# Kernel optimization log

Hardware: AMD Instinct MI355X
Metric: run time of the kernel (lower is better)

## Reference

```python
import jax, jax.numpy as jnp
import numpy as np

B, S, G, C = 4, 512, 48, 12
D = G * C            # d_model = 576, divisible by nhead=3
N = B * S * G        # 98304 graph nodes
E = N * 16           # 1572864 edges
H, FF = 3, 2048
HD = D // H
SCALE = 1.0 / float(np.sqrt(HD))


def _leaky(x):
    return jnp.where(x > 0, x, 0.2 * x)


def _ln(x, g, b):
    m = jnp.mean(x, -1, keepdims=True)
    v = jnp.var(x, -1, keepdims=True)
    return (x - m) * jax.lax.rsqrt(v + 1e-5) * g + b


def _conv(x, w, b, stride=1):
    # x: [B, Cin, L], w: [Cout, Cin, K]
    y = jax.lax.conv_general_dilated(x, w, (stride,), 'SAME',
                                     dimension_numbers=('NCH', 'OIH', 'NCH'))
    return y + b[None, :, None]


def _gat(x, src, dst, W, a_s, a_d, bias):
    # single-head GATConv (PyG defaults: self-loops already in src/dst, leaky 0.2)
    xp = x @ W.T                                            # [N, C]
    e = _leaky((xp @ a_s)[src] + (xp @ a_d)[dst])           # [E+N]
    m = jax.ops.segment_max(e, dst, num_segments=N)
    w = jnp.exp(e - m[dst])
    denom = jax.ops.segment_sum(w, dst, num_segments=N)
    alpha = w / denom[dst]
    return jax.ops.segment_sum(alpha[:, None] * xp[src], dst, num_segments=N) + bias


def _forward(edge_index, x, mask, noise,
             W_enc, a_src_enc, a_dst_enc, b_enc,
             Wq, bq, Wk, bk, Wv, bv, Wo, bo,
             ln1_g, ln1_b, W1, b1, W2, b2, ln2_g, ln2_b,
             enc1_w, enc1_b, down_w, down_b, bott_w, bott_b,
             up_w, up_b, dec_w, dec_b,
             W_dec, a_src_dec, a_dst_dec, b_dec):
    loops = jnp.arange(N)
    src = jnp.concatenate([edge_index[0], loops])
    dst = jnp.concatenate([edge_index[1], loops])
    # masked blend of observed data and imputation noise
    h = x * mask + noise * (1.0 - mask)
    h = _gat(h, src, dst, W_enc, a_src_enc, a_dst_enc, b_enc)       # [N, C]
    t = h.reshape(B, S, D)
    # TransformerEncoderLayer (post-norm, relu FFN, 3 heads)
    q = (t @ Wq.T + bq).reshape(B, S, H, HD)
    k = (t @ Wk.T + bk).reshape(B, S, H, HD)
    v = (t @ Wv.T + bv).reshape(B, S, H, HD)
    att = jax.nn.softmax(jnp.einsum('bqhd,bkhd->bhqk', q, k) * SCALE, axis=-1)
    o = jnp.einsum('bhqk,bkhd->bqhd', att, v).reshape(B, S, D) @ Wo.T + bo
    t = _ln(t + o, ln1_g, ln1_b)
    ff = jax.nn.relu(t @ W1.T + b1) @ W2.T + b2
    t = _ln(t + ff, ln2_g, ln2_b)
    # Unet1d auto-encoder over the time axis, channels = D
    y = t.transpose(0, 2, 1)                                        # [B, D, S]
    e1 = jax.nn.relu(_conv(y, enc1_w, enc1_b))                      # [B, D, S]
    d1 = jax.nn.relu(_conv(e1, down_w, down_b, 2))                  # [B, 2D, S/2]
    bt = jax.nn.relu(_conv(d1, bott_w, bott_b))                     # [B, 2D, S/2]
    up = jax.nn.relu(_conv(jnp.repeat(bt, 2, axis=2), up_w, up_b))  # [B, D, S]
    y = _conv(jnp.concatenate([up, e1], axis=1), dec_w, dec_b)      # [B, D, S]
    # GAT decoder + tanh
    h = y.transpose(0, 2, 1).reshape(N, C)
    h = _gat(h, src, dst, W_dec, a_src_dec, a_dst_dec, b_dec)
    return jnp.tanh(h)


def setup_inputs() -> dict:
    ks = iter(jax.random.split(jax.random.key(0), 64))
    def nrm(shape, s=0.2):
        return jax.random.normal(next(ks), shape, jnp.float32) * s
    return dict(
        edge_index=jax.random.randint(next(ks), (2, E), 0, N),
        x=jax.random.normal(next(ks), (N, C), jnp.float32),
        mask=(jax.random.uniform(next(ks), (N, C)) < 0.8).astype(jnp.float32),
        noise=jax.random.normal(next(ks), (N, C), jnp.float32),
        W_enc=nrm((C, C)), a_src_enc=nrm((C,)), a_dst_enc=nrm((C,)), b_enc=jnp.zeros((C,), jnp.float32),
        Wq=nrm((D, D), 0.05), bq=jnp.zeros((D,)), Wk=nrm((D, D), 0.05), bk=jnp.zeros((D,)),
        Wv=nrm((D, D), 0.05), bv=jnp.zeros((D,)), Wo=nrm((D, D), 0.05), bo=jnp.zeros((D,)),
        ln1_g=jnp.ones((D,)), ln1_b=jnp.zeros((D,)),
        W1=nrm((FF, D), 0.05), b1=jnp.zeros((FF,)), W2=nrm((D, FF), 0.05), b2=jnp.zeros((D,)),
        ln2_g=jnp.ones((D,)), ln2_b=jnp.zeros((D,)),
        enc1_w=nrm((D, D, 3), 0.03), enc1_b=jnp.zeros((D,)),
        down_w=nrm((2 * D, D, 3), 0.03), down_b=jnp.zeros((2 * D,)),
        bott_w=nrm((2 * D, 2 * D, 3), 0.02), bott_b=jnp.zeros((2 * D,)),
        up_w=nrm((D, 2 * D, 3), 0.02), up_b=jnp.zeros((D,)),
        dec_w=nrm((D, 2 * D, 3), 0.02), dec_b=jnp.zeros((D,)),
        W_dec=nrm((C, C)), a_src_dec=nrm((C,)), a_dst_dec=nrm((C,)), b_dec=jnp.zeros((C,), jnp.float32),
    )


def reference(edge_index, x, mask, noise,
              W_enc, a_src_enc, a_dst_enc, b_enc,
              Wq, bq, Wk, bk, Wv, bv, Wo, bo,
              ln1_g, ln1_b, W1, b1, W2, b2, ln2_g, ln2_b,
              enc1_w, enc1_b, down_w, down_b, bott_w, bott_b,
              up_w, up_b, dec_w, dec_b,
              W_dec, a_src_dec, a_dst_dec, b_dec):
    return _forward(edge_index, x, mask, noise,
                    W_enc, a_src_enc, a_dst_enc, b_enc,
                    Wq, bq, Wk, bk, Wv, bv, Wo, bo,
                    ln1_g, ln1_b, W1, b1, W2, b2, ln2_g, ln2_b,
                    enc1_w, enc1_b, down_w, down_b, bott_w, bott_b,
                    up_w, up_b, dec_w, dec_b,
                    W_dec, a_src_dec, a_dst_dec, b_dec)
```

## Files before the change

kernel.cpp:

```cpp
#include <hip/hip_runtime.h>
#include <hip/hip_bf16.h>
#include <math.h>

#define NN 98304
#define CC 12
#define EE 1572864
#define ETOT (EE + NN)
#define BB 4
#define SS 512
#define DD 576
#define HH 3
#define HDI 192
#define FFD 2048
#define MR (BB*SS)
#define ND (NN*CC)
#define ATT_SCALE 0.07216878364870323f
#define NB 768
#define BCAP 2560
#define BINB2 512
#define CHUNK2 3264

typedef __hip_bfloat16 bf;
typedef __attribute__((ext_vector_type(8))) short s8v;
typedef __attribute__((ext_vector_type(4))) short s4v;
typedef __attribute__((ext_vector_type(4))) float f4v;

__device__ __forceinline__ void gl16(const void* g, void* l) {
    __builtin_amdgcn_global_load_lds(
        (const __attribute__((address_space(1))) unsigned int*)g,
        (__attribute__((address_space(3))) unsigned int*)l, 16, 0, 0);
}
__device__ __forceinline__ short bfbits(float f) {
    bf t = __float2bfloat16(f);
    return *(short*)&t;
}
__device__ __forceinline__ unsigned pk2(float a, float b) {
    return (unsigned)(unsigned short)bfbits(a) |
           ((unsigned)(unsigned short)bfbits(b) << 16);
}
__device__ __forceinline__ float lo16(unsigned v) { return __uint_as_float(v << 16); }
__device__ __forceinline__ float hi16(unsigned v) { return __uint_as_float(v & 0xffff0000u); }

__global__ __launch_bounds__(256) void gat_node_k(
    const float* __restrict__ xin, const float* __restrict__ mask,
    const float* __restrict__ noise,
    const float* __restrict__ W, const float* __restrict__ a_s,
    const float* __restrict__ a_d,
    float4* __restrict__ rows, float* __restrict__ dval,
    int blend)
{
    int n = blockIdx.x * 256 + threadIdx.x;
    if (n >= NN) return;
    const float4* xr = (const float4*)(xin + (size_t)n*CC);
    float h[CC];
    float4 h0 = xr[0], h1 = xr[1], h2 = xr[2];
    h[0]=h0.x; h[1]=h0.y; h[2]=h0.z; h[3]=h0.w;
    h[4]=h1.x; h[5]=h1.y; h[6]=h1.z; h[7]=h1.w;
    h[8]=h2.x; h[9]=h2.y; h[10]=h2.z; h[11]=h2.w;
    if (blend) {
        const float4* mr = (const float4*)(mask  + (size_t)n*CC);
        const float4* nr = (const float4*)(noise + (size_t)n*CC);
        float m[CC], z[CC];
        float4 m0=mr[0],m1=mr[1],m2=mr[2], z0=nr[0],z1=nr[1],z2=nr[2];
        m[0]=m0.x;m[1]=m0.y;m[2]=m0.z;m[3]=m0.w;m[4]=m1.x;m[5]=m1.y;m[6]=m1.z;m[7]=m1.w;
        m[8]=m2.x;m[9]=m2.y;m[10]=m2.z;m[11]=m2.w;
        z[0]=z0.x;z[1]=z0.y;z[2]=z0.z;z[3]=z0.w;z[4]=z1.x;z[5]=z1.y;z[6]=z1.z;z[7]=z1.w;
        z[8]=z2.x;z[9]=z2.y;z[10]=z2.z;z[11]=z2.w;
#pragma unroll
        for (int c = 0; c < CC; ++c) h[c] = h[c]*m[c] + z[c]*(1.0f-m[c]);
    }
    float sv = 0.f, dv = 0.f;
    float o[CC];
#pragma unroll
    for (int oc = 0; oc < CC; ++oc) {
        float a = 0.f;
#pragma unroll
        for (int ic = 0; ic < CC; ++ic) a += h[ic]*W[oc*CC+ic];
        o[oc] = a;
        sv += a * a_s[oc]; dv += a * a_d[oc];
    }
    float4 r0, r1;
    r0.x = sv;
    r0.y = __uint_as_float(pk2(o[0], o[1]));
    r0.z = __uint_as_float(pk2(o[2], o[3]));
    r0.w = __uint_as_float(pk2(o[4], o[5]));
    r1.x = __uint_as_float(pk2(o[6], o[7]));
    r1.y = __uint_as_float(pk2(o[8], o[9]));
    r1.z = __uint_as_float(pk2(o[10], o[11]));
    r1.w = 0.f;
    rows[(size_t)n*2]   = r0;
    rows[(size_t)n*2+1] = r1;
    dval[n] = dv;
}

__global__ __launch_bounds__(256) void binA1_k(
    const int* __restrict__ e1, int* __restrict__ gcnt)
{
    __shared__ int lh[NB];
    const int tid = threadIdx.x;
    const int lo = blockIdx.x * CHUNK2, hi = lo + CHUNK2;
    for (int b = tid; b < NB; b += 256) lh[b] = 0;
    __syncthreads();
    for (int i = lo + tid; i < hi; i += 256) {
        int d = (i < EE) ? e1[i] : (i - EE);
        atomicAdd(&lh[d >> 7], 1);
    }
    __syncthreads();
    for (int b = tid; b < NB; b += 256)
        gcnt[(size_t)blockIdx.x*NB + b] = lh[b];
}

__global__ __launch_bounds__(512) void binscan_k(
    const int* __restrict__ gcnt, int* __restrict__ gbase, int* __restrict__ bcnt)
{
    __shared__ int sh[BINB2];
    const int b = blockIdx.x, t = threadIdx.x;
    int v = gcnt[(size_t)t*NB + b];
    sh[t] = v; __syncthreads();
    for (int off = 1; off < BINB2; off <<= 1) {
        int add = (t >= off) ? sh[t-off] : 0;
        __syncthreads();
        sh[t] += add;
        __syncthreads();
    }
    gbase[(size_t)b*BINB2 + t] = sh[t] - v;
    if (t == BINB2-1) bcnt[b] = sh[BINB2-1];
}

__global__ __launch_bounds__(256) void binA2_k(
    const int* __restrict__ e0, const int* __restrict__ e1,
    const int* __restrict__ gbase, unsigned* __restrict__ pairs)
{
    __shared__ int lbase[NB];
    __shared__ int lh[NB];
    const int tid = threadIdx.x;
    const int lo = blockIdx.x * CHUNK2, hi = lo + CHUNK2;
    for (int b = tid; b < NB; b += 256) {
        lbase[b] = gbase[(size_t)b*BINB2 + blockIdx.x];
        lh[b] = 0;
    }
    __syncthreads();
    for (int i = lo + tid; i < hi; i += 256) {
        int s, d;
        if (i < EE) { s = e0[i]; d = e1[i]; }
        else        { s = i - EE; d = s; }
        int b = d >> 7;
        int p = lbase[b] + atomicAdd(&lh[b], 1);
        if (p < BCAP)
            pairs[(size_t)b*BCAP + p] = ((unsigned)(d & 127) << 17) | (unsigned)s;
    }
}

__global__ __launch_bounds__(1024) void binB_k(
    unsigned* __restrict__ pairs, const int* __restrict__ bcnt,
    int* __restrict__ cnt, int* __restrict__ offs)
{
    __shared__ unsigned ent[BCAP];
    __shared__ int lh[128], ls[128], lc[128];
    const int b = blockIdx.x, tid = threadIdx.x;
    const int n = min(bcnt[b], BCAP);
    for (int i = tid; i < n; i += 1024) ent[i] = pairs[(size_t)b*BCAP + i];
    if (tid < 128) lh[tid] = 0;
    __syncthreads();
    for (int i = tid; i < n; i += 1024) atomicAdd(&lh[ent[i] >> 17], 1);
    __syncthreads();
    if (tid == 0) { int run = 0; for (int j = 0; j < 128; ++j) { ls[j] = run; run += lh[j]; } }
    __syncthreads();
    if (tid < 128) {
        int node = b*128 + tid;
        cnt[node]  = lh[tid];
        offs[node] = b*BCAP + ls[tid];
        lc[tid]    = ls[tid];
    }
    __syncthreads();
    for (int i = tid; i < n; i += 1024) {
        unsigned v = ent[i];
        int dl = (int)(v >> 17);
        int p = atomicAdd(&lc[dl], 1);
        pairs[(size_t)b*BCAP + p] = v & 0x1FFFFu;
    }
}

__global__ __launch_bounds__(256) void gat_agg8_k(
    const unsigned* __restrict__ pairs, const int* __restrict__ cnt,
    const int* __restrict__ offs,
    const float4* __restrict__ rows, const float* __restrict__ dval,
    const float* __restrict__ bias,
    float* __restrict__ out, bf* __restrict__ outb, int dotanh)
{
    int g = blockIdx.x*32 + (threadIdx.x >> 3);
    int l = threadIdx.x & 7;
    if (g >= NN) return;
    int beg = offs[g], m = cnt[g];
    float dv = dval[g];
    float acc[CC] = {};
    float den = 0.f;
    for (int i = l; i < m; i += 8) {
        unsigned s = pairs[beg + i];
        float4 r0 = rows[(size_t)s*2];
        float4 r1 = rows[(size_t)s*2+1];
        float e = r0.x + dv;
        e = e > 0.f ? e : 0.2f*e;
        float w = __expf(e);
        den += w;
        unsigned p01 = __float_as_uint(r0.y), p23 = __float_as_uint(r0.z);
        unsigned p45 = __float_as_uint(r0.w), p67 = __float_as_uint(r1.x);
        unsigned p89 = __float_as_uint(r1.y), pab = __float_as_uint(r1.z);
        acc[0]  += w*lo16(p01); acc[1]  += w*hi16(p01);
        acc[2]  += w*lo16(p23); acc[3]  += w*hi16(p23);
        acc[4]  += w*lo16(p45); acc[5]  += w*hi16(p45);
        acc[6]  += w*lo16(p67); acc[7]  += w*hi16(p67);
        acc[8]  += w*lo16(p89); acc[9]  += w*hi16(p89);
        acc[10] += w*lo16(pab); acc[11] += w*hi16(pab);
    }
#pragma unroll
    for (int off = 1; off < 8; off <<= 1) {
        den += __shfl_xor(den, off);
#pragma unroll
        for (int c = 0; c < CC; ++c) acc[c] += __shfl_xor(acc[c], off);
    }
    if (l == 0) {
        float inv = 1.f / den;
        float r[CC];
#pragma unroll
        for (int c = 0; c < CC; ++c) {
            r[c] = acc[c]*inv + bias[c];
            if (dotanh) r[c] = tanhf(r[c]);
        }
        if (out) {
            float4* orow = (float4*)(out + (size_t)g*CC);
            orow[0] = make_float4(r[0],r[1],r[2],r[3]);
            orow[1] = make_float4(r[4],r[5],r[6],r[7]);
            orow[2] = make_float4(r[8],r[9],r[10],r[11]);
        }
        if (outb) {
            s4v* brow = (s4v*)(outb + (size_t)g*CC);
            s4v b0, b1, b2;
            b0[0]=bfbits(r[0]); b0[1]=bfbits(r[1]); b0[2]=bfbits(r[2]); b0[3]=bfbits(r[3]);
            b1[0]=bfbits(r[4]); b1[1]=bfbits(r[5]); b1[2]=bfbits(r[6]); b1[3]=bfbits(r[7]);
            b2[0]=bfbits(r[8]); b2[1]=bfbits(r[9]); b2[2]=bfbits(r[10]); b2[3]=bfbits(r[11]);
            brow[0]=b0; brow[1]=b1; brow[2]=b2;
        }
    }
}

template<int TBM>
__global__ __launch_bounds__(256) void gemm_bt(
    const bf* __restrict__ A, const bf* __restrict__ B,
    const float* __restrict__ bias, float* __restrict__ Cf, bf* __restrict__ Cb,
    int K, int lda, int ldb, int ldc,
    long long sA1, long long sA2, long long sB1, long long sB2,
    long long sC1, long long sC2, int bdiv, long long sBias,
    float scale, int relu, int vtmode)
{
    constexpr int MI = TBM/32;
    __shared__ bf As[TBM*32];
    __shared__ bf Bs[64*32];
    const int tid = threadIdx.x, lane = tid & 63, wave = tid >> 6;
    const int z = blockIdx.z, z1 = z / bdiv, z2 = z % bdiv;
    const bf* Ab = A + z1*sA1 + z2*sA2;
    const bf* Bb = B + z1*sB1 + z2*sB2;
    const int bm = blockIdx.y * TBM, bn = blockIdx.x * 64;
    const int l4 = lane >> 2;
    const int swz0 = (l4 >> 1) & 3;
    const int lc = (((lane & 3) ^ swz0) * 8);
    const int arow0 = wave*(TBM/4) + l4;
    const int brow  = wave*16 + l4;
    const int wm = wave >> 1, wn = wave & 1;
    const int fr = lane & 15;
    const int gsw = (((lane >> 4) ^ ((fr >> 1) & 3)) * 8);
    f4v acc[MI][2] = {};

    for (int k0 = 0; k0 < K; k0 += 32) {
        gl16(Ab + (size_t)(bm + arow0)*lda + k0 + lc, As + wave*(TBM/4)*32);
        if constexpr (TBM == 128)
            gl16(Ab + (size_t)(bm + arow0 + 16)*lda + k0 + lc, As + wave*1024 + 512);
        gl16(Bb + (size_t)(bn + brow )*ldb + k0 + lc, Bs + wave*512);
        __syncthreads();
        s8v af[MI], bfv[2];
#pragma unroll
        for (int mi = 0; mi < MI; ++mi)
            af[mi] = *(const s8v*)&As[(wm*(TBM/2) + mi*16 + fr)*32 + gsw];
#pragma unroll
        for (int nj = 0; nj < 2; ++nj)
            bfv[nj] = *(const s8v*)&Bs[(wn*32 + nj*16 + fr)*32 + gsw];
#pragma unroll
        for (int mi = 0; mi < MI; ++mi)
#pragma unroll
            for (int nj = 0; nj < 2; ++nj)
                acc[mi][nj] = __builtin_amdgcn_mfma_f32_16x16x32_bf16(
                    af[mi], bfv[nj], acc[mi][nj], 0, 0, 0);
        __syncthreads();
    }

    const float* bp = bias ? bias + z1*sBias : nullptr;
    if (vtmode && z1 == 2) {
        bf* vt = Cb + 2*sC1;
#pragma unroll
        for (int mi = 0; mi < MI; ++mi) {
#pragma unroll
            for (int nj = 0; nj < 2; ++nj) {
                int col = bn + wn*32 + nj*16 + fr;
                float bv = bp ? bp[col] : 0.f;
                int row0 = bm + wm*(TBM/2) + mi*16 + (lane>>4)*4;
                int b = row0 >> 9, s0 = row0 & 511;
                int h = col / HDI, dd = col - h*HDI;
                s4v pk;
#pragma unroll
                for (int r = 0; r < 4; ++r)
                    pk[r] = bfbits(acc[mi][nj][r] + bv);
                *(s4v*)&vt[((size_t)((b*HH + h)*HDI + dd))*SS + s0] = pk;
            }
        }
        return;
    }
    float* Cfb = Cf ? Cf + z1*sC1 + z2*sC2 : nullptr;
    bf*    Cbb = Cb ? Cb + z1*sC1 + z2*sC2 : nullptr;
#pragma unroll
    for (int mi = 0; mi < MI; ++mi) {
#pragma unroll
        for (int nj = 0; nj < 2; ++nj) {
            int col = bn + wn*32 + nj*16 + fr;
            float bv = bp ? bp[col] : 0.f;
#pragma unroll
            for (int r = 0; r < 4; ++r) {
                int row = bm + wm*(TBM/2) + mi*16 + (lane>>4)*4 + r;
                float vv = (acc[mi][nj][r] + bv) * scale;
                if (relu) vv = fmaxf(vv, 0.f);
                if (Cfb) Cfb[(size_t)row*ldc + col] = vv;
                if (Cbb) Cbb[(size_t)row*ldc + col] = __float2bfloat16(vv);
            }
        }
    }
}

template<int CIN, int MODE>
__global__ __launch_bounds__(256) void conv_bt(
    const bf* __restrict__ A0, const bf* __restrict__ A1,
    const bf* __restrict__ Bw, float* __restrict__ Cpart,
    int K, int M, int N, int Lout, int Lin, int splitk)
{
    __shared__ bf As[64*32];
    __shared__ bf Bs[64*32];
    const int tid = threadIdx.x, lane = tid & 63, wave = tid >> 6;
    const int bm = blockIdx.y * 64, bn = blockIdx.x * 64;
    const int kchunk = K / splitk;
    const int kbeg = blockIdx.z * kchunk, kend = kbeg + kchunk;
    const int l4 = lane >> 2;
    const int swz0 = (l4 >> 1) & 3;
    const int lc = (((lane & 3) ^ swz0) * 8);
    const int arow = bm + wave*16 + l4;
    const int brow = bn + wave*16 + l4;
    const int ab = arow / Lout, al = arow % Lout;
    const int wm = wave >> 1, wn = wave & 1;
    const int fr = lane & 15;
    const int gsw = (((lane >> 4) ^ ((fr >> 1) & 3)) * 8);
    f4v acc[2][2] = {};

    for (int k0 = kbeg; k0 < kend; k0 += 32) {
        int kk  = k0 / CIN;
        int ci0 = k0 - kk*CIN;
        int row;
        if constexpr (MODE == 1)      row = 2*al + kk + 1;
        else if constexpr (MODE == 2) row = (al + kk + 1) >> 1;
        else                          row = al + kk;
        const bf* src;
        if constexpr (MODE == 3) {
            constexpr int CH = CIN/2;
            bool lohalf = ci0 < CH;
            src = (lohalf ? A0 : A1)
                + ((size_t)(ab*(Lin+2) + row))*CH + (lohalf ? ci0 : ci0 - CH);
        } else {
            src = A0 + ((size_t)(ab*(Lin+2) + row))*CIN + ci0;
        }
        gl16(src + lc, As + wave*512);
        gl16(Bw + (size_t)brow*K + k0 + lc, Bs + wave*512);
        __syncthreads();
        s8v af[2], bfv[2];
#pragma unroll
        for (int mi = 0; mi < 2; ++mi)
            af[mi] = *(const s8v*)&As[(wm*32 + mi*16 + fr)*32 + gsw];
#pragma unroll
        for (int nj = 0; nj < 2; ++nj)
            bfv[nj] = *(const s8v*)&Bs[(wn*32 + nj*16 + fr)*32 + gsw];
#pragma unroll
        for (int mi = 0; mi < 2; ++mi)
#pragma unroll
            for (int nj = 0; nj < 2; ++nj)
                acc[mi][nj] = __builtin_amdgcn_mfma_f32_16x16x32_bf16(
                    af[mi], bfv[nj], acc[mi][nj], 0, 0, 0);
        __syncthreads();
    }

    float* Cp = Cpart + (size_t)blockIdx.z * M * N;
#pragma unroll
    for (int mi = 0; mi < 2; ++mi)
#pragma unroll
        for (int nj = 0; nj < 2; ++nj) {
            int col = bn + wn*32 + nj*16 + fr;
#pragma unroll
            for (int r = 0; r < 4; ++r) {
                int row = bm + wm*32 + mi*16 + (lane>>4)*4 + r;
                Cp[(size_t)row*N + col] = acc[mi][nj][r];
            }
        }
}

__global__ __launch_bounds__(256) void convepi_k(
    const float* __restrict__ part, const float* __restrict__ bias,
    bf* __restrict__ outb, float* __restrict__ outf,
    int M, int N, int Lout, int relu, int nsplit)
{
    int total = M * (N >> 3);
    int i = blockIdx.x*256 + threadIdx.x;
    if (i >= total) return;
    int c8 = (i % (N >> 3)) * 8;
    int row = i / (N >> 3);
    float v[8];
#pragma unroll
    for (int j = 0; j < 8; ++j) v[j] = bias[c8+j];
    for (int z = 0; z < nsplit; ++z) {
        const float* p = part + (size_t)z*M*N + (size_t)row*N + c8;
#pragma unroll
        for (int j = 0; j < 8; ++j) v[j] += p[j];
    }
    if (relu) {
#pragma unroll
        for (int j = 0; j < 8; ++j) v[j] = fmaxf(v[j], 0.f);
    }
    if (outb) {
        int b = row / Lout, l = row % Lout;
        s8v pk;
#pragma unroll
        for (int j = 0; j < 8; ++j) pk[j] = bfbits(v[j]);
        *(s8v*)&outb[((size_t)(b*(Lout+2) + l + 1))*N + c8] = pk;
    }
    if (outf) {
        float4* o = (float4*)(outf + (size_t)row*N + c8);
        o[0] = make_float4(v[0],v[1],v[2],v[3]);
        o[1] = make_float4(v[4],v[5],v[6],v[7]);
    }
}

struct PJob { int type; const float* src; void* dst; int a; int b; };
struct PJobs { PJob j[14]; };
__global__ __launch_bounds__(256) void prep_k(PJobs J)
{
    PJob jb = J.j[blockIdx.y];
    if (jb.type == 0) {
        for (int i = blockIdx.x*256 + threadIdx.x; i < jb.a; i += gridDim.x*256) {
            float4 v = ((const float4*)jb.src)[i];
            s4v p;
            p[0]=bfbits(v.x); p[1]=bfbits(v.y); p[2]=bfbits(v.z); p[3]=bfbits(v.w);
            ((s4v*)jb.dst)[i] = p;
        }
    } else if (jb.type == 1) {
        for (int i = blockIdx.x*256 + threadIdx.x; i < jb.a; i += gridDim.x*256)
            ((float4*)jb.dst)[i] = ((const float4*)jb.src)[i];
    } else {
        int n8 = BB * 2 * (jb.b >> 3);
        for (int i = blockIdx.x*256 + threadIdx.x; i < n8; i += gridDim.x*256) {
            int c8 = i % (jb.b >> 3); int r = i / (jb.b >> 3);
            int bb = r >> 1; int row = (r & 1) ? (jb.a + 1) : 0;
            s8v z = {0,0,0,0,0,0,0,0};
            *(s8v*)&((bf*)jb.dst)[((size_t)(bb*(jb.a+2) + row))*jb.b + c8*8] = z;
        }
    }
}

struct WJob { const float* w; bf* wT; int Cout; int Cin; };
struct WJobs { WJob j[5]; };
__global__ __launch_bounds__(256) void wtrans5_k(WJobs J)
{
    WJob jb = J.j[blockIdx.y];
    int n8 = jb.Cout * 3 * (jb.Cin >> 3);
    for (int i = blockIdx.x*256 + threadIdx.x; i < n8; i += gridDim.x*256) {
        int c8 = i % (jb.Cin >> 3); int r = i / (jb.Cin >> 3);
        int kk = r % 3; int co = r / 3;
        int ci = c8 * 8;
        s8v ov;
#pragma unroll
        for (int j = 0; j < 8; ++j)
            ov[j] = bfbits(jb.w[((size_t)co*jb.Cin + ci + j)*3 + kk]);
        *(s8v*)&jb.wT[(size_t)co*3*jb.Cin + (size_t)kk*jb.Cin + ci] = ov;
    }
}

__global__ __launch_bounds__(256) void softmax_k(
    const float* __restrict__ S, bf* __restrict__ P)
{
    int row = blockIdx.x; size_t base = (size_t)row * SS;
    int tid = threadIdx.x;
    __shared__ float red[256];
    float v0 = S[base+tid], v1 = S[base+tid+256];
    red[tid] = fmaxf(v0, v1); __syncthreads();
    for (int off = 128; off > 0; off >>= 1) {
        if (tid < off) red[tid] = fmaxf(red[tid], red[tid+off]);
        __syncthreads();
    }
    float mx = red[0]; __syncthreads();
    float e0 = __expf(v0-mx), e1 = __expf(v1-mx);
    red[tid] = e0+e1; __syncthreads();
    for (int off = 128; off > 0; off >>= 1) {
        if (tid < off) red[tid] += red[tid+off];
        __syncthreads();
    }
    float inv = 1.f / red[0];
    P[base+tid]     = __float2bfloat16(e0*inv);
    P[base+tid+256] = __float2bfloat16(e1*inv);
}

__global__ __launch_bounds__(256) void ln_k(
    const float* __restrict__ a, const float* __restrict__ r,
    const float* __restrict__ g, const float* __restrict__ be,
    float* __restrict__ out, bf* __restrict__ ob, int padout)
{
    int row = blockIdx.x; int tid = threadIdx.x;
    __shared__ float red[256], red2[256];
    size_t base = (size_t)row * DD;
    size_t base2 = padout ? ((size_t)(row + 2*(row/SS) + 1))*DD : base;
    float x0 = a[base+tid]      + r[base+tid];
    float x1 = a[base+tid+256]  + r[base+tid+256];
    float x2 = (tid < 64) ? (a[base+tid+512] + r[base+tid+512]) : 0.f;
    float s  = x0+x1+x2;
    float s2 = x0*x0 + x1*x1 + x2*x2;
    red[tid] = s; red2[tid] = s2; __syncthreads();
    for (int off = 128; off > 0; off >>= 1) {
        if (tid < off) { red[tid] += red[tid+off]; red2[tid] += red2[tid+off]; }
        __syncthreads();
    }
    float mean = red[0] / (float)DD;
    float var  = red2[0] / (float)DD - mean*mean;
    float inv = rsqrtf(var + 1e-5f);
    float y0 = (x0-mean)*inv*g[tid]     + be[tid];
    float y1 = (x1-mean)*inv*g[tid+256] + be[tid+256];
    if (out) { out[base+tid] = y0; out[base+tid+256] = y1; }
    if (ob)  { ob[base2+tid] = __float2bfloat16(y0); ob[base2+tid+256] = __float2bfloat16(y1); }
    if (tid < 64) {
        float y2 = (x2-mean)*inv*g[tid+512] + be[tid+512];
        if (out) out[base+tid+512] = y2;
        if (ob)  ob[base2+tid+512] = __float2bfloat16(y2);
    }
}

extern "C" void kernel_launch(void* const* d_in, const int* in_sizes, int n_in,
                              void* d_out, int out_size, void* d_ws, size_t ws_size,
                              hipStream_t stream)
{
    const int*   edge   = (const int*)  d_in[0];
    const float* x      = (const float*)d_in[1];
    const float* mask   = (const float*)d_in[2];
    const float* noise  = (const float*)d_in[3];
    const float* W_enc  = (const float*)d_in[4];
    const float* asrc_e = (const float*)d_in[5];
    const float* adst_e = (const float*)d_in[6];
    const float* b_enc  = (const float*)d_in[7];
    const float* Wq = (const float*)d_in[8];  const float* bq = (const float*)d_in[9];
    const float* Wk = (const float*)d_in[10]; const float* bk = (const float*)d_in[11];
    const float* Wv = (const float*)d_in[12]; const float* bv = (const float*)d_in[13];
    const float* Wo = (const float*)d_in[14]; const float* bo = (const float*)d_in[15];
    const float* ln1g = (const float*)d_in[16]; const float* ln1b = (const float*)d_in[17];
    const float* W1 = (const float*)d_in[18]; const float* b1 = (const float*)d_in[19];
    const float* W2 = (const float*)d_in[20]; const float* b2 = (const float*)d_in[21];
    const float* ln2g = (const float*)d_in[22]; const float* ln2b = (const float*)d_in[23];
    const float* enc1_w = (const float*)d_in[24]; const float* enc1_b = (const float*)d_in[25];
    const float* down_w = (const float*)d_in[26]; const float* down_b = (const float*)d_in[27];
    const float* bott_w = (const float*)d_in[28]; const float* bott_b = (const float*)d_in[29];
    const float* up_w   = (const float*)d_in[30]; const float* up_b   = (const float*)d_in[31];
    const float* dec_w  = (const float*)d_in[32]; const float* dec_b  = (const float*)d_in[33];
    const float* W_dec  = (const float*)d_in[34];
    const float* asrc_d = (const float*)d_in[35];
    const float* adst_d = (const float*)d_in[36];
    const float* b_dec  = (const float*)d_in[37];
    float* out = (float*)d_out;

    float* ws = (float*)d_ws;
    float4*   rows  = (float4*)ws;
    float*    dval  = ws + 786432;
    int*      cnt   = (int*)(ws + 884736);
    int*      offs  = (int*)(ws + 983040);
    unsigned* pairs = (unsigned*)(ws + 1376256);
    int*      bcnt  = (int*)(ws + 3342336);
    float*    t     = ws + 3343360;
    bf*       tb    = (bf*)(ws + 4523008);
    bf*       qb    = (bf*)(ws + 5112832);
    bf*       kb    = (bf*)(ws + 5702656);
    bf*       vb    = (bf*)(ws + 6292480);
    float*    big   = ws + 6882304;
    int*      gcnt  = (int*)big;
    int*      gbase = (int*)(big + 393216);
    float*    scores = big;
    bf*       Pb    = (bf*)(big + 3145728);
    bf*       wTbott = (bf*)big;
    float*    o     = ws + 11600896;
    float*    parts = ws + 11600896;
    float*    t1    = ws + 12780544;
    bf*       t1b   = (bf*)(ws + 13960192);
    bf*       ff1b  = (bf*)(ws + 14550016);
    bf*       t2p   = (bf*)(ws + 16647168);
    bf*       e1p   = (bf*)(ws + 17239296);
    bf*       d1p   = (bf*)(ws + 17831424);
    bf*       btbp  = (bf*)(ws + 18425856);
    bf*       upp   = (bf*)(ws + 19020288);
    float*    dec   = ws + 19612416;
    bf*       wTb   = (bf*)(ws + 20792064);
    bf*       Wqb   = (bf*)(ws + 21787392);
    bf*       Wkb   = (bf*)(ws + 21953280);
    bf*       Wvb   = (bf*)(ws + 22119168);
    bf*       Wob   = (bf*)(ws + 22285056);
    bf*       W1b   = (bf*)(ws + 22450944);
    bf*       W2b   = (bf*)(ws + 23040768);
    float*    biasQKV = ws + 23630592;
    bf*       vt    = vb;
    bf*       attnO = qb;
    bf*       wTenc  = wTb;
    bf*       wTdown = (bf*)t;
    bf*       wTup   = kb;
    bf*       wTdec  = tb;

    const int* e0 = edge;
    const int* e1i = edge + EE;

    binA1_k<<<BINB2, 256, 0, stream>>>(e1i, gcnt);
    binscan_k<<<NB, BINB2, 0, stream>>>(gcnt, gbase, bcnt);
    binA2_k<<<BINB2, 256, 0, stream>>>(e0, e1i, gbase, pairs);
    binB_k<<<NB, 1024, 0, stream>>>(pairs, bcnt, cnt, offs);

    {
        PJobs J;
        J.j[0]  = { 0, Wq, Wqb, DD*DD/4, 0 };
        J.j[1]  = { 0, Wk, Wkb, DD*DD/4, 0 };
        J.j[2]  = { 0, Wv, Wvb, DD*DD/4, 0 };
        J.j[3]  = { 0, Wo, Wob, DD*DD/4, 0 };
        J.j[4]  = { 0, W1, W1b, FFD*DD/4, 0 };
        J.j[5]  = { 0, W2, W2b, FFD*DD/4, 0 };
        J.j[6]  = { 1, bq, biasQKV,        DD/4, 0 };
        J.j[7]  = { 1, bk, biasQKV + DD,   DD/4, 0 };
        J.j[8]  = { 1, bv, biasQKV + 2*DD, DD/4, 0 };
        J.j[9]  = { 2, nullptr, t2p,  512, 576 };
        J.j[10] = { 2, nullptr, e1p,  512, 576 };
        J.j[11] = { 2, nullptr, d1p,  256, 1152 };
        J.j[12] = { 2, nullptr, btbp, 256, 1152 };
        J.j[13] = { 2, nullptr, upp,  512, 576 };
        prep_k<<<dim3(576, 14), 256, 0, stream>>>(J);
    }

    gat_node_k<<<NN/256, 256, 0, stream>>>(x, mask, noise, W_enc, asrc_e, adst_e,
                                           rows, dval, 1);
    gat_agg8_k<<<NN/32, 256, 0, stream>>>(pairs, cnt, offs, rows, dval, b_enc,
                                          t, tb, 0);

    gemm_bt<128><<<dim3(9,16,3), 256, 0, stream>>>(tb, Wqb, biasQKV, nullptr, qb,
        DD, DD, DD, DD,
        0,0, (long long)DD*DD,0, (long long)MR*DD,0, 1, DD, 1.f, 0, 1);
    gemm_bt<128><<<dim3(8,4,12), 256, 0, stream>>>(qb, kb, nullptr, scores, nullptr,
        HDI, DD, DD, SS,
        (long long)SS*DD, HDI, (long long)SS*DD, HDI,
        3LL*SS*SS, (long long)SS*SS, HH, 0, ATT_SCALE, 0, 0);
    softmax_k<<<12*SS, 256, 0, stream>>>(scores, Pb);
    gemm_bt<64><<<dim3(3,8,12), 256, 0, stream>>>(Pb, vt, nullptr, nullptr, attnO,
        SS, SS, SS, DD,
        3LL*SS*SS, (long long)SS*SS, 3LL*HDI*SS, (long long)HDI*SS,
        (long long)SS*DD, HDI, HH, 0, 1.f, 0, 0);
    gemm_bt<64><<<dim3(9,32,1), 256, 0, stream>>>(attnO, Wob, bo, o, nullptr,
        DD, DD, DD, DD, 0,0,0,0,0,0, 1, 0, 1.f, 0, 0);
    ln_k<<<MR, 256, 0, stream>>>(t, o, ln1g, ln1b, t1, t1b, 0);
    gemm_bt<128><<<dim3(32,16,1), 256, 0, stream>>>(t1b, W1b, b1, nullptr, ff1b,
        DD, DD, DD, FFD, 0,0,0,0,0,0, 1, 0, 1.f, 1, 0);
    gemm_bt<64><<<dim3(9,32,1), 256, 0, stream>>>(ff1b, W2b, b2, o, nullptr,
        FFD, FFD, FFD, DD, 0,0,0,0,0,0, 1, 0, 1.f, 0, 0);
    ln_k<<<MR, 256, 0, stream>>>(t1, o, ln2g, ln2b, nullptr, t2p, 1);

    {
        WJobs W5;
        W5.j[0] = { enc1_w, wTenc,  576,  576 };
        W5.j[1] = { down_w, wTdown, 1152, 576 };
        W5.j[2] = { bott_w, wTbott, 1152, 1152 };
        W5.j[3] = { up_w,   wTup,   576,  1152 };
        W5.j[4] = { dec_w,  wTdec,  576,  1152 };
        wtrans5_k<<<dim3(1024, 5), 256, 0, stream>>>(W5);
    }
    conv_bt<576,0><<<dim3(9,32,3), 256, 0, stream>>>(t2p, nullptr, wTenc, parts,
        1728, 2048, 576, 512, 512, 3);
    convepi_k<<<576, 256, 0, stream>>>(parts, enc1_b, e1p, nullptr, 2048, 576, 512, 1, 3);
    conv_bt<576,1><<<dim3(18,16,3), 256, 0, stream>>>(e1p, nullptr, wTdown, parts,
        1728, 1024, 1152, 256, 512, 3);
    convepi_k<<<576, 256, 0, stream>>>(parts, down_b, d1p, nullptr, 1024, 1152, 256, 1, 3);
    conv_bt<1152,0><<<dim3(18,16,4), 256, 0, stream>>>(d1p, nullptr, wTbott, parts,
        3456, 1024, 1152, 256, 256, 4);
    convepi_k<<<576, 256, 0, stream>>>(parts, bott_b, btbp, nullptr, 1024, 1152, 256, 1, 4);
    conv_bt<1152,2><<<dim3(9,32,4), 256, 0, stream>>>(btbp, nullptr, wTup, parts,
        3456, 2048, 576, 512, 256, 4);
    convepi_k<<<576, 256, 0, stream>>>(parts, up_b, upp, nullptr, 2048, 576, 512, 1, 4);
    conv_bt<1152,3><<<dim3(9,32,4), 256, 0, stream>>>(upp, e1p, wTdec, parts,
        3456, 2048, 576, 512, 512, 4);
    convepi_k<<<576, 256, 0, stream>>>(parts, dec_b, nullptr, dec, 2048, 576, 512, 0, 4);

    gat_node_k<<<NN/256, 256, 0, stream>>>(dec, nullptr, nullptr, W_dec, asrc_d, adst_d,
                                           rows, dval, 0);
    gat_agg8_k<<<NN/32, 256, 0, stream>>>(pairs, cnt, offs, rows, dval, b_dec,
                                          out, nullptr, 1);
}
```

Measured before the change: 353.2 us.

## Replace split-K conv GEMMs with 32-row tiles and fused bias/ReLU epilogue

The five Conv1d GEMMs drop split-K with float partial buffers and separate reduction/epilogue kernels. Each now runs as a single kernel over the full K with 32-row tiles, applying bias, ReLU and the bf16 padded store directly. The gemm_bt template also gains a 32-row tile variant, used for the attention PV, Wo and W2 GEMMs to raise block counts. This removes the partial-sum traffic and five launches, at the cost of half as many MFMAs per block and two idle waves during A-tile loads.

```diff
diff --git a/kernel.cpp b/kernel.cpp
--- a/kernel.cpp
+++ b/kernel.cpp
@@ -264,7 +264,7 @@
     const int l4 = lane >> 2;
     const int swz0 = (l4 >> 1) & 3;
     const int lc = (((lane & 3) ^ swz0) * 8);
-    const int arow0 = wave*(TBM/4) + l4;
+    const int arow0 = wave*((TBM==128)?32:16) + l4;
     const int brow  = wave*16 + l4;
     const int wm = wave >> 1, wn = wave & 1;
     const int fr = lane & 15;
@@ -272,9 +272,15 @@
     f4v acc[MI][2] = {};
 
     for (int k0 = 0; k0 < K; k0 += 32) {
-        gl16(Ab + (size_t)(bm + arow0)*lda + k0 + lc, As + wave*(TBM/4)*32);
-        if constexpr (TBM == 128)
+        if constexpr (TBM == 32) {
+            if (wave < 2)
+                gl16(Ab + (size_t)(bm + arow0)*lda + k0 + lc, As + wave*512);
+        } else if constexpr (TBM == 64) {
+            gl16(Ab + (size_t)(bm + arow0)*lda + k0 + lc, As + wave*512);
+        } else {
+            gl16(Ab + (size_t)(bm + arow0)*lda + k0 + lc, As + wave*1024);
             gl16(Ab + (size_t)(bm + arow0 + 16)*lda + k0 + lc, As + wave*1024 + 512);
+        }
         gl16(Bb + (size_t)(bn + brow )*ldb + k0 + lc, Bs + wave*512);
         __syncthreads();
         s8v af[MI], bfv[2];
@@ -335,17 +341,16 @@
 }
 
 template<int CIN, int MODE>
-__global__ __launch_bounds__(256) void conv_bt(
+__global__ __launch_bounds__(256) void conv32_k(
     const bf* __restrict__ A0, const bf* __restrict__ A1,
-    const bf* __restrict__ Bw, float* __restrict__ Cpart,
-    int K, int M, int N, int Lout, int Lin, int splitk)
-{
-    __shared__ bf As[64*32];
+    const bf* __restrict__ Bw, const float* __restrict__ bias,
+    bf* __restrict__ outb, float* __restrict__ outf,
+    int K, int N, int Lout, int Lin, int relu)
+{
+    __shared__ bf As[32*32];
     __shared__ bf Bs[64*32];
     const int tid = threadIdx.x, lane = tid & 63, wave = tid >> 6;
-    const int bm = blockIdx.y * 64, bn = blockIdx.x * 64;
-    const int kchunk = K / splitk;
-    const int kbeg = blockIdx.z * kchunk, kend = kbeg + kchunk;
+    const int bm = blockIdx.y * 32, bn = blockIdx.x * 64;
     const int l4 = lane >> 2;
     const int swz0 = (l4 >> 1) & 3;
     const int lc = (((lane & 3) ^ swz0) * 8);
@@ -355,90 +360,52 @@
     const int wm = wave >> 1, wn = wave & 1;
     const int fr = lane & 15;
     const int gsw = (((lane >> 4) ^ ((fr >> 1) & 3)) * 8);
-    f4v acc[2][2] = {};
-
-    for (int k0 = kbeg; k0 < kend; k0 += 32) {
+    f4v acc[2] = {};
+
+    for (int k0 = 0; k0 < K; k0 += 32) {
         int kk  = k0 / CIN;
         int ci0 = k0 - kk*CIN;
-        int row;
-        if constexpr (MODE == 1)      row = 2*al + kk + 1;
-        else if constexpr (MODE == 2) row = (al + kk + 1) >> 1;
-        else                          row = al + kk;
-        const bf* src;
-        if constexpr (MODE == 3) {
-            constexpr int CH = CIN/2;
-            bool lohalf = ci0 < CH;
-            src = (lohalf ? A0 : A1)
-                + ((size_t)(ab*(Lin+2) + row))*CH + (lohalf ? ci0 : ci0 - CH);
-        } else {
-            src = A0 + ((size_t)(ab*(Lin+2) + row))*CIN + ci0;
-        }
-        gl16(src + lc, As + wave*512);
+        if (wave < 2) {
+            int row;
+            if constexpr (MODE == 1)      row = 2*al + kk + 1;
+            else if constexpr (MODE == 2) row = (al + kk + 1) >> 1;
+            else                          row = al + kk;
+            const bf* src;
+            if constexpr (MODE == 3) {
+                constexpr int CH = CIN/2;
+                bool lohalf = ci0 < CH;
+                src = (lohalf ? A0 : A1)
+                    + ((size_t)(ab*(Lin+2) + row))*CH + (lohalf ? ci0 : ci0 - CH);
+            } else {
+                src = A0 + ((size_t)(ab*(Lin+2) + row))*CIN + ci0;
+            }
+            gl16(src + lc, As + wave*512);
+        }
         gl16(Bw + (size_t)brow*K + k0 + lc, Bs + wave*512);
         __syncthreads();
-        s8v af[2], bfv[2];
-#pragma unroll
-        for (int mi = 0; mi < 2; ++mi)
-            af[mi] = *(const s8v*)&As[(wm*32 + mi*16 + fr)*32 + gsw];
-#pragma unroll
-        for (int nj = 0; nj < 2; ++nj)
-            bfv[nj] = *(const s8v*)&Bs[(wn*32 + nj*16 + fr)*32 + gsw];
-#pragma unroll
-        for (int mi = 0; mi < 2; ++mi)
-#pragma unroll
-            for (int nj = 0; nj < 2; ++nj)
-                acc[mi][nj] = __builtin_amdgcn_mfma_f32_16x16x32_bf16(
-                    af[mi], bfv[nj], acc[mi][nj], 0, 0, 0);
-        __syncthreads();
-    }
-
-    float* Cp = Cpart + (size_t)blockIdx.z * M * N;
-#pragma unroll
-    for (int mi = 0; mi < 2; ++mi)
-#pragma unroll
-        for (int nj = 0; nj < 2; ++nj) {
-            int col = bn + wn*32 + nj*16 + fr;
-#pragma unroll
-            for (int r = 0; r < 4; ++r) {
-                int row = bm + wm*32 + mi*16 + (lane>>4)*4 + r;
-                Cp[(size_t)row*N + col] = acc[mi][nj][r];
+        s8v af = *(const s8v*)&As[(wm*16 + fr)*32 + gsw];
+        s8v b0 = *(const s8v*)&Bs[(wn*32 + fr)*32 + gsw];
+        s8v b1 = *(const s8v*)&Bs[(wn*32 + 16 + fr)*32 + gsw];
+        acc[0] = __builtin_amdgcn_mfma_f32_16x16x32_bf16(af, b0, acc[0], 0, 0, 0);
+        acc[1] = __builtin_amdgcn_mfma_f32_16x16x32_bf16(af, b1, acc[1], 0, 0, 0);
+        __syncthreads();
+    }
+
+#pragma unroll
+    for (int nj = 0; nj < 2; ++nj) {
+        int col = bn + wn*32 + nj*16 + fr;
+        float bv = bias[col];
+#pragma unroll
+        for (int r = 0; r < 4; ++r) {
+            int row = bm + wm*16 + (lane>>4)*4 + r;
+            float vv = acc[nj][r] + bv;
+            if (relu) vv = fmaxf(vv, 0.f);
+            if (outb) {
+                int b = row / Lout, l = row % Lout;
+                outb[((size_t)(b*(Lout+2) + l + 1))*N + col] = __float2bfloat16(vv);
             }
-        }
-}
-
-__global__ __launch_bounds__(256) void convepi_k(
-    const float* __restrict__ part, const float* __restrict__ bias,
-    bf* __restrict__ outb, float* __restrict__ outf,
-    int M, int N, int Lout, int relu, int nsplit)
-{
-    int total = M * (N >> 3);
-    int i = blockIdx.x*256 + threadIdx.x;
-    if (i >= total) return;
-    int c8 = (i % (N >> 3)) * 8;
-    int row = i / (N >> 3);
-    float v[8];
-#pragma unroll
-    for (int j = 0; j < 8; ++j) v[j] = bias[c8+j];
-    for (int z = 0; z < nsplit; ++z) {
-        const float* p = part + (size_t)z*M*N + (size_t)row*N + c8;
-#pragma unroll
-        for (int j = 0; j < 8; ++j) v[j] += p[j];
-    }
-    if (relu) {
-#pragma unroll
-        for (int j = 0; j < 8; ++j) v[j] = fmaxf(v[j], 0.f);
-    }
-    if (outb) {
-        int b = row / Lout, l = row % Lout;
-        s8v pk;
-#pragma unroll
-        for (int j = 0; j < 8; ++j) pk[j] = bfbits(v[j]);
-        *(s8v*)&outb[((size_t)(b*(Lout+2) + l + 1))*N + c8] = pk;
-    }
-    if (outf) {
-        float4* o = (float4*)(outf + (size_t)row*N + c8);
-        o[0] = make_float4(v[0],v[1],v[2],v[3]);
-        o[1] = make_float4(v[4],v[5],v[6],v[7]);
+            if (outf) outf[(size_t)row*N + col] = vv;
+        }
     }
 }
 
@@ -593,7 +560,6 @@
     bf*       Pb    = (bf*)(big + 3145728);
     bf*       wTbott = (bf*)big;
     float*    o     = ws + 11600896;
-    float*    parts = ws + 11600896;
     float*    t1    = ws + 12780544;
     bf*       t1b   = (bf*)(ws + 13960192);
     bf*       ff1b  = (bf*)(ws + 14550016);
@@ -658,16 +624,16 @@
         (long long)SS*DD, HDI, (long long)SS*DD, HDI,
         3LL*SS*SS, (long long)SS*SS, HH, 0, ATT_SCALE, 0, 0);
     softmax_k<<<12*SS, 256, 0, stream>>>(scores, Pb);
-    gemm_bt<64><<<dim3(3,8,12), 256, 0, stream>>>(Pb, vt, nullptr, nullptr, attnO,
+    gemm_bt<32><<<dim3(3,16,12), 256, 0, stream>>>(Pb, vt, nullptr, nullptr, attnO,
         SS, SS, SS, DD,
         3LL*SS*SS, (long long)SS*SS, 3LL*HDI*SS, (long long)HDI*SS,
         (long long)SS*DD, HDI, HH, 0, 1.f, 0, 0);
-    gemm_bt<64><<<dim3(9,32,1), 256, 0, stream>>>(attnO, Wob, bo, o, nullptr,
+    gemm_bt<32><<<dim3(9,64,1), 256, 0, stream>>>(attnO, Wob, bo, o, nullptr,
         DD, DD, DD, DD, 0,0,0,0,0,0, 1, 0, 1.f, 0, 0);
     ln_k<<<MR, 256, 0, stream>>>(t, o, ln1g, ln1b, t1, t1b, 0);
     gemm_bt<128><<<dim3(32,16,1), 256, 0, stream>>>(t1b, W1b, b1, nullptr, ff1b,
         DD, DD, DD, FFD, 0,0,0,0,0,0, 1, 0, 1.f, 1, 0);
-    gemm_bt<64><<<dim3(9,32,1), 256, 0, stream>>>(ff1b, W2b, b2, o, nullptr,
+    gemm_bt<32><<<dim3(9,64,1), 256, 0, stream>>>(ff1b, W2b, b2, o, nullptr,
         FFD, FFD, FFD, DD, 0,0,0,0,0,0, 1, 0, 1.f, 0, 0);
     ln_k<<<MR, 256, 0, stream>>>(t1, o, ln2g, ln2b, nullptr, t2p, 1);
 
@@ -680,21 +646,16 @@
         W5.j[4] = { dec_w,  wTdec,  576,  1152 };
         wtrans5_k<<<dim3(1024, 5), 256, 0, stream>>>(W5);
     }
-    conv_bt<576,0><<<dim3(9,32,3), 256, 0, stream>>>(t2p, nullptr, wTenc, parts,
-        1728, 2048, 576, 512, 512, 3);
-    convepi_k<<<576, 256, 0, stream>>>(parts, enc1_b, e1p, nullptr, 2048, 576, 512, 1, 3);
-    conv_bt<576,1><<<dim3(18,16,3), 256, 0, stream>>>(e1p, nullptr, wTdown, parts,
-        1728, 1024, 1152, 256, 512, 3);
-    convepi_k<<<576, 256, 0, stream>>>(parts, down_b, d1p, nullptr, 1024, 1152, 256, 1, 3);
-    conv_bt<1152,0><<<dim3(18,16,4), 256, 0, stream>>>(d1p, nullptr, wTbott, parts,
-        3456, 1024, 1152, 256, 256, 4);
-    convepi_k<<<576, 256, 0, stream>>>(parts, bott_b, btbp, nullptr, 1024, 1152, 256, 1, 4);
-    conv_bt<1152,2><<<dim3(9,32,4), 256, 0, stream>>>(btbp, nullptr, wTup, parts,
-        3456, 2048, 576, 512, 256, 4);
-    convepi_k<<<576, 256, 0, stream>>>(parts, up_b, upp, nullptr, 2048, 576, 512, 1, 4);
-    conv_bt<1152,3><<<dim3(9,32,4), 256, 0, stream>>>(upp, e1p, wTdec, parts,
-        3456, 2048, 576, 512, 512, 4);
-    convepi_k<<<576, 256, 0, stream>>>(parts, dec_b, nullptr, dec, 2048, 576, 512, 0, 4);
+    conv32_k<576,0><<<dim3(9,64), 256, 0, stream>>>(t2p, nullptr, wTenc, enc1_b,
+        e1p, nullptr, 1728, 576, 512, 512, 1);
+    conv32_k<576,1><<<dim3(18,32), 256, 0, stream>>>(e1p, nullptr, wTdown, down_b,
+        d1p, nullptr, 1728, 1152, 256, 512, 1);
+    conv32_k<1152,0><<<dim3(18,32), 256, 0, stream>>>(d1p, nullptr, wTbott, bott_b,
+        btbp, nullptr, 3456, 1152, 256, 256, 1);
+    conv32_k<1152,2><<<dim3(9,64), 256, 0, stream>>>(btbp, nullptr, wTup, up_b,
+        upp, nullptr, 3456, 576, 512, 256, 1);
+    conv32_k<1152,3><<<dim3(9,64), 256, 0, stream>>>(upp, e1p, wTdec, dec_b,
+        nullptr, dec, 3456, 576, 512, 512, 0);
 
     gat_node_k<<<NN/256, 256, 0, stream>>>(dec, nullptr, nullptr, W_dec, asrc_d, adst_d,
                                            rows, dval, 0);
```

New measurement: 437.1 us. 23.8% more time.

## Fuse QK^T score GEMM with row softmax into one attention kernel

Applied to the files above, without the earlier changes.

Replaces the separate score GEMM, which wrote fp32 scores to global memory, and the row-softmax kernel with a single kernel. Each block computes a 32-query by 512-key score tile with MFMA, then does the max and sum reductions across waves in registers and LDS. It writes bf16 probabilities directly. This removes the fp32 score round trip and one launch, but uses only 192 blocks and reloads the full K for every query tile.

```diff
diff --git a/kernel.cpp b/kernel.cpp
--- a/kernel.cpp
+++ b/kernel.cpp
@@ -334,6 +334,116 @@
     }
 }
 
+__global__ __launch_bounds__(256) void qk_softmax_k(
+    const bf* __restrict__ q, const bf* __restrict__ k, bf* __restrict__ P)
+{
+    __shared__ bf Qs[32*32];
+    __shared__ bf Ks[512*32];
+    __shared__ float redm[32][4];
+    __shared__ float reds[32][4];
+    const int tid = threadIdx.x, lane = tid & 63, wave = tid >> 6;
+    const int bh = blockIdx.y;
+    const int b = bh / HH, h = bh % HH;
+    const int q0 = blockIdx.x * 32;
+    const bf* Qp = q + (size_t)(b*SS + q0)*DD + h*HDI;
+    const bf* Kp = k + (size_t)(b*SS)*DD + h*HDI;
+    const int l4 = lane >> 2;
+    const int swz0 = (l4 >> 1) & 3;
+    const int lc = (((lane & 3) ^ swz0) * 8);
+    const int fr = lane & 15, q4 = lane >> 4;
+    const int gsw = ((q4 ^ ((fr >> 1) & 3)) * 8);
+    f4v acc[2][8] = {};
+
+    for (int k0 = 0; k0 < HDI; k0 += 32) {
+        if (wave < 2)
+            gl16(Qp + (size_t)(wave*16 + l4)*DD + k0 + lc, Qs + wave*512);
+#pragma unroll
+        for (int it = 0; it < 8; ++it) {
+            int srow = it*64 + wave*16 + l4;
+            gl16(Kp + (size_t)srow*DD + k0 + lc, Ks + (it*64 + wave*16)*32);
+        }
+        __syncthreads();
+        s8v af[2], bfv[8];
+#pragma unroll
+        for (int mi = 0; mi < 2; ++mi)
+            af[mi] = *(const s8v*)&Qs[(mi*16 + fr)*32 + gsw];
+#pragma unroll
+        for (int nj = 0; nj < 8; ++nj)
+            bfv[nj] = *(const s8v*)&Ks[(wave*128 + nj*16 + fr)*32 + gsw];
+#pragma unroll
+        for (int mi = 0; mi < 2; ++mi)
+#pragma unroll
+            for (int nj = 0; nj < 8; ++nj)
+                acc[mi][nj] = __builtin_amdgcn_mfma_f32_16x16x32_bf16(
+                    af[mi], bfv[nj], acc[mi][nj], 0, 0, 0);
+        __syncthreads();
+    }
+
+#pragma unroll
+    for (int mi = 0; mi < 2; ++mi)
+#pragma unroll
+        for (int nj = 0; nj < 8; ++nj)
+            acc[mi][nj] *= ATT_SCALE;
+
+    float mx[2][4];
+#pragma unroll
+    for (int mi = 0; mi < 2; ++mi)
+#pragma unroll
+        for (int r = 0; r < 4; ++r) {
+            float m = acc[mi][0][r];
+#pragma unroll
+            for (int nj = 1; nj < 8; ++nj) m = fmaxf(m, acc[mi][nj][r]);
+#pragma unroll
+            for (int off = 1; off < 16; off <<= 1)
+                m = fmaxf(m, __shfl_xor(m, off));
+            if (fr == 0) redm[mi*16 + q4*4 + r][wave] = m;
+            mx[mi][r] = m;
+        }
+    __syncthreads();
+#pragma unroll
+    for (int mi = 0; mi < 2; ++mi)
+#pragma unroll
+        for (int r = 0; r < 4; ++r) {
+            int row = mi*16 + q4*4 + r;
+            mx[mi][r] = fmaxf(fmaxf(redm[row][0], redm[row][1]),
+                              fmaxf(redm[row][2], redm[row][3]));
+        }
+    float sm[2][4];
+#pragma unroll
+    for (int mi = 0; mi < 2; ++mi)
+#pragma unroll
+        for (int r = 0; r < 4; ++r) {
+            float s = 0.f;
+#pragma unroll
+            for (int nj = 0; nj < 8; ++nj) {
+                float e = __expf(acc[mi][nj][r] - mx[mi][r]);
+                acc[mi][nj][r] = e;
+                s += e;
+            }
+#pragma unroll
+            for (int off = 1; off < 16; off <<= 1)
+                s += __shfl_xor(s, off);
+            if (fr == 0) reds[mi*16 + q4*4 + r][wave] = s;
+            sm[mi][r] = s;
+        }
+    __syncthreads();
+    bf* Pp = P + (size_t)bh*SS*SS;
+#pragma unroll
+    for (int mi = 0; mi < 2; ++mi)
+#pragma unroll
+        for (int r = 0; r < 4; ++r) {
+            int row = mi*16 + q4*4 + r;
+            float tot = reds[row][0] + reds[row][1] + reds[row][2] + reds[row][3];
+            float inv = 1.f / tot;
+#pragma unroll
+            for (int nj = 0; nj < 8; ++nj) {
+                int col = wave*128 + nj*16 + fr;
+                Pp[(size_t)(q0 + row)*SS + col] =
+                    __float2bfloat16(acc[mi][nj][r] * inv);
+            }
+        }
+}
+
 template<int CIN, int MODE>
 __global__ __launch_bounds__(256) void conv_bt(
     const bf* __restrict__ A0, const bf* __restrict__ A1,
@@ -484,30 +594,6 @@
             ov[j] = bfbits(jb.w[((size_t)co*jb.Cin + ci + j)*3 + kk]);
         *(s8v*)&jb.wT[(size_t)co*3*jb.Cin + (size_t)kk*jb.Cin + ci] = ov;
     }
-}
-
-__global__ __launch_bounds__(256) void softmax_k(
-    const float* __restrict__ S, bf* __restrict__ P)
-{
-    int row = blockIdx.x; size_t base = (size_t)row * SS;
-    int tid = threadIdx.x;
-    __shared__ float red[256];
-    float v0 = S[base+tid], v1 = S[base+tid+256];
-    red[tid] = fmaxf(v0, v1); __syncthreads();
-    for (int off = 128; off > 0; off >>= 1) {
-        if (tid < off) red[tid] = fmaxf(red[tid], red[tid+off]);
-        __syncthreads();
-    }
-    float mx = red[0]; __syncthreads();
-    float e0 = __expf(v0-mx), e1 = __expf(v1-mx);
-    red[tid] = e0+e1; __syncthreads();
-    for (int off = 128; off > 0; off >>= 1) {
-        if (tid < off) red[tid] += red[tid+off];
-        __syncthreads();
-    }
-    float inv = 1.f / red[0];
-    P[base+tid]     = __float2bfloat16(e0*inv);
-    P[base+tid+256] = __float2bfloat16(e1*inv);
 }
 
 __global__ __launch_bounds__(256) void ln_k(
@@ -589,9 +675,8 @@
     float*    big   = ws + 6882304;
     int*      gcnt  = (int*)big;
     int*      gbase = (int*)(big + 393216);
-    float*    scores = big;
-    bf*       Pb    = (bf*)(big + 3145728);
-    bf*       wTbott = (bf*)big;
+    bf*       Pb    = (bf*)big;
+    bf*       wTbott = (bf*)(big + 1572864);
     float*    o     = ws + 11600896;
     float*    parts = ws + 11600896;
     float*    t1    = ws + 12780544;
@@ -653,11 +738,7 @@
     gemm_bt<128><<<dim3(9,16,3), 256, 0, stream>>>(tb, Wqb, biasQKV, nullptr, qb,
         DD, DD, DD, DD,
         0,0, (long long)DD*DD,0, (long long)MR*DD,0, 1, DD, 1.f, 0, 1);
-    gemm_bt<128><<<dim3(8,4,12), 256, 0, stream>>>(qb, kb, nullptr, scores, nullptr,
-        HDI, DD, DD, SS,
-        (long long)SS*DD, HDI, (long long)SS*DD, HDI,
-        3LL*SS*SS, (long long)SS*SS, HH, 0, ATT_SCALE, 0, 0);
-    softmax_k<<<12*SS, 256, 0, stream>>>(scores, Pb);
+    qk_softmax_k<<<dim3(16,12), 256, 0, stream>>>(qb, kb, Pb);
     gemm_bt<64><<<dim3(3,8,12), 256, 0, stream>>>(Pb, vt, nullptr, nullptr, attnO,
         SS, SS, SS, DD,
         3LL*SS*SS, (long long)SS*SS, 3LL*HDI*SS, (long long)HDI*SS,
```

Result: no change. 348.2 us (-1.4%).
